# Kernel optimization log

Hardware: AMD Instinct MI355X
Metric: run time of the kernel (lower is better)

## Reference

```python
import jax, jax.numpy as jnp
import numpy as np

SCALE = 0.08838834764831845  # head_dim ** -0.5
NUM_HEADS = 32
NUM_KV_HEADS = 8
HEAD_DIM = 128
PAGE_SIZE = 16


def setup_inputs() -> dict:
    key = jax.random.key(0)
    k1, k2 = jax.random.split(key)
    B = 32
    L0_PAGES = 256        # shared prefix: 4096 tokens
    L1_PAGES = 64         # per-seq chunk: 1024 tokens
    L2_PAGES = 32         # per-seq suffix: 512 tokens
    P = L0_PAGES + B * L1_PAGES + B * L2_PAGES  # 3328 pages
    q = jax.random.normal(k1, (B, NUM_HEADS * HEAD_DIM), jnp.float32)
    # paged KV cache, layout [page, k/v, page_size, kv_heads, head_dim]
    kv_cache = jax.random.normal(k2, (P, 2, PAGE_SIZE, NUM_KV_HEADS, HEAD_DIM), jnp.float32)
    shared_page_idx = jnp.arange(L0_PAGES, dtype=jnp.int32)
    seq1_page_idx = (L0_PAGES + jnp.arange(B * L1_PAGES, dtype=jnp.int32)).reshape(B, L1_PAGES)
    seq2_page_idx = (L0_PAGES + B * L1_PAGES + jnp.arange(B * L2_PAGES, dtype=jnp.int32)).reshape(B, L2_PAGES)
    return {"q": q, "kv_cache": kv_cache, "shared_page_idx": shared_page_idx,
            "seq1_page_idx": seq1_page_idx, "seq2_page_idx": seq2_page_idx}


def _softmax_attn(scores, V, av_eq):
    # scores: [..., L]; returns (out, lse) with a single stable pass
    m = scores.max(axis=-1, keepdims=True)
    e = jnp.exp(scores - m)
    denom = e.sum(axis=-1)
    out = jnp.einsum(av_eq, e, V) / denom[..., None]
    lse = m[..., 0] + jnp.log(denom)
    return out, lse


def _merge_state(oa, sa, ob, sb):
    # flashinfer.merge_state: LSE-weighted combination of attention states
    s = jnp.logaddexp(sa, sb)
    o = oa * jnp.exp(sa - s)[..., None] + ob * jnp.exp(sb - s)[..., None]
    return o, s


def _forward(q, kv_cache, shared_page_idx, seq1_page_idx, seq2_page_idx):
    B = q.shape[0]
    G = NUM_HEADS // NUM_KV_HEADS  # GQA group size = 4
    # q -> [B, Hkv, G, D]
    q4 = q.reshape(B, NUM_KV_HEADS, G, HEAD_DIM)

    # level 0: shared pages -> [L0, Hkv, D]
    K0 = kv_cache[shared_page_idx, 0].reshape(-1, NUM_KV_HEADS, HEAD_DIM)
    V0 = kv_cache[shared_page_idx, 1].reshape(-1, NUM_KV_HEADS, HEAD_DIM)
    s0 = jnp.einsum('bkgd,lkd->bkgl', q4, K0) * SCALE
    out, lse = _softmax_attn(s0, V0, 'bkgl,lkd->bkgd')

    # levels 1 and 2: per-sequence paged KV -> [B, Li, Hkv, D]
    for idx in (seq1_page_idx, seq2_page_idx):
        Ki = kv_cache[idx, 0].reshape(B, -1, NUM_KV_HEADS, HEAD_DIM)
        Vi = kv_cache[idx, 1].reshape(B, -1, NUM_KV_HEADS, HEAD_DIM)
        si = jnp.einsum('bkgd,blkd->bkgl', q4, Ki) * SCALE
        oi, li = _softmax_attn(si, Vi, 'bkgl,blkd->bkgd')
        out, lse = _merge_state(out, lse, oi, li)

    return out.reshape(B, NUM_HEADS * HEAD_DIM)


def reference(q, kv_cache, shared_page_idx, seq1_page_idx, seq2_page_idx):
    return _forward(q, kv_cache, shared_page_idx, seq1_page_idx, seq2_page_idx)
```

## Files before the change

### kernel.cpp

```cpp
#include <hip/hip_runtime.h>
#include <stdint.h>


namespace {
constexpr int kG = 4, kD = 128;
constexpr float kQS = 0.08838834764831845f * 1.4426950408889634f;
constexpr int kNChunk = 32;
constexpr int kNSplit = 3;
constexpr int kNSrc = kNChunk + kNSplit;
constexpr size_t kOParts = (size_t)kNSrc * 32 * 8 * 4 * 128;
constexpr size_t kMLB = kOParts;
constexpr size_t kWsFloats = kOParts + (size_t)kNSrc * 32 * 8 * 4 * 2;
}

__device__ __forceinline__ float wave_max(float v) {
#pragma unroll
    for (int off = 1; off < 64; off <<= 1) v = fmaxf(v, __shfl_xor(v, off));
    return v;
}
__device__ __forceinline__ float wave_sum(float v) {
#pragma unroll
    for (int off = 1; off < 64; off <<= 1) v += __shfl_xor(v, off);
    return v;
}
__device__ __forceinline__ int kslot(int s, int t) { return s ^ (t & 31); }
__device__ __forceinline__ int vslot(int s, int t) {
    return s ^ (((t << 1) & 31) | ((t >> 4) & 1));
}

__global__ __launch_bounds__(512, 2)
void l0_kernel(const float* __restrict__ q, const float* __restrict__ kv,
               const int* __restrict__ sp0, float* __restrict__ ws)
{
    __shared__ __align__(16) float q_lds[32 * kG * kD];
    __shared__ __align__(16) float buf[2 * 64 * kD];
    __shared__ int pgs[8];

    const int h = blockIdx.x & 7;
    const int chunk = blockIdx.x >> 3;
    const int tid = threadIdx.x;
    const int w = tid >> 6, lane = tid & 63;

    {
        const int j0 = tid * 32;
        const int b = j0 >> 9, r = j0 & 511;
        const float4* src = (const float4*)(q + (size_t)b * 4096 + h * 512 + r);
        float4* dst = (float4*)&q_lds[j0];
#pragma unroll
        for (int u = 0; u < 8; ++u) {
            float4 v = src[u];
            v.x *= kQS; v.y *= kQS; v.z *= kQS; v.w *= kQS;
            dst[u] = v;
        }
    }
    if (tid < 8) pgs[tid] = sp0[chunk * 8 + tid];

    for (int pass = 0; pass < 2; ++pass) {
        float m[8], l[8], acc[8][8];
#pragma unroll
        for (int r = 0; r < 8; ++r) {
            m[r] = -1e30f; l[r] = 0.f;
#pragma unroll
            for (int e = 0; e < 8; ++e) acc[r][e] = 0.f;
        }

        for (int st = 0; st < 2; ++st) {
            __syncthreads();
            {
                const int t = tid >> 3;
                const int sg = (tid & 7) * 4;
                const int pg = pgs[st * 4 + (t >> 4)];
                const float* gk = kv + (size_t)pg * 32768 + (size_t)(t & 15) * 1024 + h * 128;
#pragma unroll
                for (int j = 0; j < 4; ++j) {
                    const int s = sg + j;
                    *(float4*)&buf[t * 128 + (kslot(s, t) << 2)] =
                        *(const float4*)(gk + s * 4);
                    *(float4*)&buf[8192 + t * 128 + (vslot(s, t) << 2)] =
                        *(const float4*)(gk + 16384 + s * 4);
                }
            }
            __syncthreads();

            const int sw = lane;
            float s[8] = {0.f,0.f,0.f,0.f,0.f,0.f,0.f,0.f};
#pragma unroll
            for (int c = 0; c < 16; ++c) {
                float4 ka = *(const float4*)&buf[lane * 128 + (kslot(2 * c, sw) << 2)];
                float4 kb = *(const float4*)&buf[lane * 128 + (kslot(2 * c + 1, sw) << 2)];
#pragma unroll
                for (int r = 0; r < 8; ++r) {
                    const int b = w * 4 + pass * 2 + (r >> 2);
                    const float* qp = &q_lds[(b * 4 + (r & 3)) * 128 + c * 8];
                    float4 qa = *(const float4*)qp;
                    float4 qb = *(const float4*)(qp + 4);
                    s[r] += ka.x * qa.x + ka.y * qa.y + ka.z * qa.z + ka.w * qa.w
                          + kb.x * qb.x + kb.y * qb.y + kb.z * qb.z + kb.w * qb.w;
                }
            }
            float p[8];
#pragma unroll
            for (int r = 0; r < 8; ++r) {
                float mt = wave_max(s[r]);
                float mn = fmaxf(m[r], mt);
                float alpha = exp2f(m[r] - mn);
                p[r] = exp2f(s[r] - mn);
                m[r] = mn;
                l[r] = l[r] * alpha + wave_sum(p[r]);
#pragma unroll
                for (int e = 0; e < 8; ++e) acc[r][e] *= alpha;
            }
            const int tq = lane >> 4, dg = lane & 15;
#pragma unroll
            for (int j = 0; j < 16; ++j) {
                const int t = tq * 16 + j;
                float4 va = *(const float4*)&buf[8192 + t * 128 + (vslot(2 * dg, t) << 2)];
                float4 vb = *(const float4*)&buf[8192 + t * 128 + (vslot(2 * dg + 1, t) << 2)];
#pragma unroll
                for (int r = 0; r < 8; ++r) {
                    float pj = __shfl(p[r], t);
                    acc[r][0] = fmaf(pj, va.x, acc[r][0]);
                    acc[r][1] = fmaf(pj, va.y, acc[r][1]);
                    acc[r][2] = fmaf(pj, va.z, acc[r][2]);
                    acc[r][3] = fmaf(pj, va.w, acc[r][3]);
                    acc[r][4] = fmaf(pj, vb.x, acc[r][4]);
                    acc[r][5] = fmaf(pj, vb.y, acc[r][5]);
                    acc[r][6] = fmaf(pj, vb.z, acc[r][6]);
                    acc[r][7] = fmaf(pj, vb.w, acc[r][7]);
                }
            }
        }

#pragma unroll
        for (int r = 0; r < 8; ++r)
#pragma unroll
            for (int e = 0; e < 8; ++e) {
                float v = acc[r][e];
                v += __shfl_xor(v, 16);
                v += __shfl_xor(v, 32);
                acc[r][e] = v;
            }
        if (lane < 16) {
            const int dg = lane;
#pragma unroll
            for (int r = 0; r < 8; ++r) {
                const int b = w * 4 + pass * 2 + (r >> 2);
                const size_t ob = ((((size_t)chunk * 32 + b) * 8 + h) * 4 + (r & 3)) * 128 + dg * 8;
                *(float4*)&ws[ob]     = make_float4(acc[r][0], acc[r][1], acc[r][2], acc[r][3]);
                *(float4*)&ws[ob + 4] = make_float4(acc[r][4], acc[r][5], acc[r][6], acc[r][7]);
            }
        }
        if (lane == 0) {
#pragma unroll
            for (int r = 0; r < 8; ++r) {
                const int b = w * 4 + pass * 2 + (r >> 2);
                const size_t idx = (((size_t)chunk * 32 + b) * 8 + h) * 4 + (r & 3);
                ws[kMLB + 2 * idx] = m[r];
                ws[kMLB + 2 * idx + 1] = l[r];
            }
        }
    }
}

__global__ __launch_bounds__(512, 4)
void seq_kernel(const float* __restrict__ q, const float* __restrict__ kv,
                const int* __restrict__ sp1, const int* __restrict__ sp2,
                float* __restrict__ ws)
{
    __shared__ __align__(16) float qs[kG * kD];
    __shared__ int plist[32];
    __shared__ __align__(16) float wacc[8][kG * kD];
    __shared__ float wm[8][kG], wl[8][kG];

    const int bid = blockIdx.x;
    const int split = bid >> 8;
    const int b = (bid & 255) >> 3;
    const int h = bid & 7;
    const int tid = threadIdx.x;

    {
        const int g = tid >> 7, d = tid & 127;
        qs[g * 128 + d] = q[(size_t)b * 4096 + h * 512 + g * 128 + d] * kQS;
    }
    if (tid < 32) {
        const int gi = split * 32 + tid;
        plist[tid] = (gi < 64) ? sp1[b * 64 + gi] : sp2[b * 32 + (gi - 64)];
    }
    __syncthreads();

    const int w = tid >> 6, lane = tid & 63;
    const int ts = lane >> 4, dg = lane & 15;
    const int page = plist[w * 4 + ts];
    const size_t poff = (size_t)page * 32768u;
    const float* Kp = kv + poff + (size_t)(lane & 15) * 1024u + h * 128;
    const float* Vp = kv + poff + 16384u + h * 128 + dg * 8;
    const float4* qv4 = (const float4*)qs;

    float s[kG] = {0.f, 0.f, 0.f, 0.f};
#pragma unroll
    for (int c = 0; c < 16; ++c) {
        float4 ka = *(const float4*)(Kp + c * 8);
        float4 kb = *(const float4*)(Kp + c * 8 + 4);
#pragma unroll
        for (int g = 0; g < kG; ++g) {
            float4 qa = qv4[g * 32 + c * 2];
            float4 qb = qv4[g * 32 + c * 2 + 1];
            s[g] += ka.x * qa.x + ka.y * qa.y + ka.z * qa.z + ka.w * qa.w
                  + kb.x * qb.x + kb.y * qb.y + kb.z * qb.z + kb.w * qb.w;
        }
    }
    float m[kG], p[kG], l[kG], acc[kG][8];
#pragma unroll
    for (int g = 0; g < kG; ++g) {
        m[g] = wave_max(s[g]);
        p[g] = exp2f(s[g] - m[g]);
        l[g] = wave_sum(p[g]);
#pragma unroll
        for (int e = 0; e < 8; ++e) acc[g][e] = 0.f;
    }
#pragma unroll
    for (int j = 0; j < 16; ++j) {
        const int t = ts * 16 + j;
        float4 va = *(const float4*)(Vp + (size_t)j * 1024u);
        float4 vb = *(const float4*)(Vp + (size_t)j * 1024u + 4);
#pragma unroll
        for (int g = 0; g < kG; ++g) {
            float pj = __shfl(p[g], t);
            acc[g][0] = fmaf(pj, va.x, acc[g][0]);
            acc[g][1] = fmaf(pj, va.y, acc[g][1]);
            acc[g][2] = fmaf(pj, va.z, acc[g][2]);
            acc[g][3] = fmaf(pj, va.w, acc[g][3]);
            acc[g][4] = fmaf(pj, vb.x, acc[g][4]);
            acc[g][5] = fmaf(pj, vb.y, acc[g][5]);
            acc[g][6] = fmaf(pj, vb.z, acc[g][6]);
            acc[g][7] = fmaf(pj, vb.w, acc[g][7]);
        }
    }
#pragma unroll
    for (int g = 0; g < kG; ++g)
#pragma unroll
        for (int e = 0; e < 8; ++e) {
            float v = acc[g][e];
            v += __shfl_xor(v, 16);
            v += __shfl_xor(v, 32);
            acc[g][e] = v;
        }
    if (lane < 16) {
#pragma unroll
        for (int g = 0; g < kG; ++g) {
            *(float4*)&wacc[w][g * 128 + dg * 8]     = make_float4(acc[g][0], acc[g][1], acc[g][2], acc[g][3]);
            *(float4*)&wacc[w][g * 128 + dg * 8 + 4] = make_float4(acc[g][4], acc[g][5], acc[g][6], acc[g][7]);
        }
        if (lane == 0)
#pragma unroll
            for (int g = 0; g < kG; ++g) { wm[w][g] = m[g]; wl[w][g] = l[g]; }
    }
    __syncthreads();

    {
        const int g = tid >> 7, d = tid & 127;
        float mstar = wm[0][g];
#pragma unroll
        for (int ww = 1; ww < 8; ++ww) mstar = fmaxf(mstar, wm[ww][g]);
        float numer = 0.f, denom = 0.f;
#pragma unroll
        for (int ww = 0; ww < 8; ++ww) {
            float sc = exp2f(wm[ww][g] - mstar);
            denom = fmaf(sc, wl[ww][g], denom);
            numer = fmaf(sc, wacc[ww][g * 128 + d], numer);
        }
        const size_t src = (size_t)(kNChunk + split);
        const size_t ob = (((src * 32 + b) * 8 + h) * 4 + g) * 128 + d;
        ws[ob] = numer;
        if (d == 0) {
            const size_t idx = ((src * 32 + b) * 8 + h) * 4 + g;
            ws[kMLB + 2 * idx] = mstar;
            ws[kMLB + 2 * idx + 1] = denom;
        }
    }
}

__global__ __launch_bounds__(512, 4)
void merge_kernel(const float* __restrict__ ws, float* __restrict__ out)
{
    __shared__ float sm[kNSrc][4], sl[kNSrc][4];
    const int b = blockIdx.x >> 3, h = blockIdx.x & 7;
    const int tid = threadIdx.x;
    if (tid < kNSrc * 4) {
        const int src = tid >> 2, g = tid & 3;
        const size_t idx = ((((size_t)src * 32 + b) * 8 + h) * 4 + g);
        sm[src][g] = ws[kMLB + 2 * idx];
        sl[src][g] = ws[kMLB + 2 * idx + 1];
    }
    __syncthreads();
    const int g = tid >> 7, d = tid & 127;
    float mstar = -1e30f;
#pragma unroll
    for (int s = 0; s < kNSrc; ++s) mstar = fmaxf(mstar, sm[s][g]);
    float numer = 0.f, denom = 0.f;
#pragma unroll 7
    for (int s = 0; s < kNSrc; ++s) {
        const float sc = exp2f(sm[s][g] - mstar);
        denom = fmaf(sc, sl[s][g], denom);
        const size_t ob = ((((size_t)s * 32 + b) * 8 + h) * 4 + g) * 128 + d;
        numer = fmaf(sc, ws[ob], numer);
    }
    out[(size_t)b * 4096 + h * 512 + g * 128 + d] = numer / denom;
}

__global__ __launch_bounds__(512, 2)
void fallback_kernel(const float* __restrict__ q, const float* __restrict__ kv,
                     const int* __restrict__ sp0, const int* __restrict__ sp1,
                     const int* __restrict__ sp2, float* __restrict__ out)
{
    __shared__ __align__(16) float qs[kG * kD];
    __shared__ int plist[352];
    __shared__ __align__(16) float wacc[8][kG * kD];
    __shared__ float wm[8][kG], wl[8][kG];
    const int b = blockIdx.x >> 3, h = blockIdx.x & 7;
    const int tid = threadIdx.x;
    {
        const int g = tid >> 7, d = tid & 127;
        qs[g * 128 + d] = q[(size_t)b * 4096 + h * 512 + g * 128 + d] * kQS;
    }
    if (tid < 352) {
        int pg;
        if (tid < 256)      pg = sp0[tid];
        else if (tid < 320) pg = sp1[b * 64 + (tid - 256)];
        else                pg = sp2[b * 32 + (tid - 320)];
        plist[tid] = pg;
    }
    __syncthreads();
    const int w = tid >> 6, lane = tid & 63;
    const int ts = lane >> 4, dg = lane & 15;
    const float4* qv4 = (const float4*)qs;
    float m[kG], l[kG], acc[kG][8];
#pragma unroll
    for (int g = 0; g < kG; ++g) {
        m[g] = -1e30f; l[g] = 0.f;
#pragma unroll
        for (int e = 0; e < 8; ++e) acc[g][e] = 0.f;
    }
    for (int tile = 0; tile < 11; ++tile) {
        const int page = plist[w * 44 + tile * 4 + ts];
        const size_t poff = (size_t)page * 32768u;
        const float* Kp = kv + poff + (size_t)(lane & 15) * 1024u + h * 128;
        const float* Vp = kv + poff + 16384u + h * 128 + dg * 8;
        float s[kG] = {0.f, 0.f, 0.f, 0.f};
#pragma unroll
        for (int c = 0; c < 16; ++c) {
            float4 ka = *(const float4*)(Kp + c * 8);
            float4 kb = *(const float4*)(Kp + c * 8 + 4);
#pragma unroll
            for (int g = 0; g < kG; ++g) {
                float4 qa = qv4[g * 32 + c * 2];
                float4 qb = qv4[g * 32 + c * 2 + 1];
                s[g] += ka.x * qa.x + ka.y * qa.y + ka.z * qa.z + ka.w * qa.w
                      + kb.x * qb.x + kb.y * qb.y + kb.z * qb.z + kb.w * qb.w;
            }
        }
        float p[kG];
#pragma unroll
        for (int g = 0; g < kG; ++g) {
            float mt = wave_max(s[g]);
            float mn = fmaxf(m[g], mt);
            float alpha = exp2f(m[g] - mn);
            p[g] = exp2f(s[g] - mn);
            m[g] = mn;
            l[g] = l[g] * alpha + wave_sum(p[g]);
#pragma unroll
            for (int e = 0; e < 8; ++e) acc[g][e] *= alpha;
        }
#pragma unroll
        for (int j = 0; j < 16; ++j) {
            const int t = ts * 16 + j;
            float4 va = *(const float4*)(Vp + (size_t)j * 1024u);
            float4 vb = *(const float4*)(Vp + (size_t)j * 1024u + 4);
#pragma unroll
            for (int g = 0; g < kG; ++g) {
                float pj = __shfl(p[g], t);
                acc[g][0] = fmaf(pj, va.x, acc[g][0]);
                acc[g][1] = fmaf(pj, va.y, acc[g][1]);
                acc[g][2] = fmaf(pj, va.z, acc[g][2]);
                acc[g][3] = fmaf(pj, va.w, acc[g][3]);
                acc[g][4] = fmaf(pj, vb.x, acc[g][4]);
                acc[g][5] = fmaf(pj, vb.y, acc[g][5]);
                acc[g][6] = fmaf(pj, vb.z, acc[g][6]);
                acc[g][7] = fmaf(pj, vb.w, acc[g][7]);
            }
        }
    }
#pragma unroll
    for (int g = 0; g < kG; ++g)
#pragma unroll
        for (int e = 0; e < 8; ++e) {
            float v = acc[g][e];
            v += __shfl_xor(v, 16);
            v += __shfl_xor(v, 32);
            acc[g][e] = v;
        }
    if (lane < 16) {
#pragma unroll
        for (int g = 0; g < kG; ++g) {
            *(float4*)&wacc[w][g * 128 + dg * 8]     = make_float4(acc[g][0], acc[g][1], acc[g][2], acc[g][3]);
            *(float4*)&wacc[w][g * 128 + dg * 8 + 4] = make_float4(acc[g][4], acc[g][5], acc[g][6], acc[g][7]);
        }
        if (lane == 0)
#pragma unroll
            for (int g = 0; g < kG; ++g) { wm[w][g] = m[g]; wl[w][g] = l[g]; }
    }
    __syncthreads();
    {
        const int g = tid >> 7, d = tid & 127;
        float mstar = wm[0][g];
#pragma unroll
        for (int ww = 1; ww < 8; ++ww) mstar = fmaxf(mstar, wm[ww][g]);
        float numer = 0.f, denom = 0.f;
#pragma unroll
        for (int ww = 0; ww < 8; ++ww) {
            float sc = exp2f(wm[ww][g] - mstar);
            denom = fmaf(sc, wl[ww][g], denom);
            numer = fmaf(sc, wacc[ww][g * 128 + d], numer);
        }
        out[(size_t)b * 4096 + h * 512 + g * 128 + d] = numer / denom;
    }
}

extern "C" void kernel_launch(void* const* d_in, const int* in_sizes, int n_in,
                              void* d_out, int out_size, void* d_ws, size_t ws_size,
                              hipStream_t stream) {
    const float* q  = (const float*)d_in[0];
    const float* kv = (const float*)d_in[1];
    const int* sp0 = (const int*)d_in[2];
    const int* sp1 = (const int*)d_in[3];
    const int* sp2 = (const int*)d_in[4];
    float* out = (float*)d_out;
    float* ws = (float*)d_ws;
    if (ws_size >= kWsFloats * sizeof(float)) {
        hipLaunchKernelGGL(l0_kernel,    dim3(256), dim3(512), 0, stream, q, kv, sp0, ws);
        hipLaunchKernelGGL(seq_kernel,   dim3(768), dim3(512), 0, stream, q, kv, sp1, sp2, ws);
        hipLaunchKernelGGL(merge_kernel, dim3(256), dim3(512), 0, stream, ws, out);
    } else {
        hipLaunchKernelGGL(fallback_kernel, dim3(256), dim3(512), 0, stream,
                           q, kv, sp0, sp1, sp2, out);
    }
}
```

Before: 690.0 us.

## Fuse shared-prefix and per-sequence attention into one interleaved kernel launch

Combines the level-0 shared-prefix kernel and the per-sequence split kernel into a single 1280-block launch, interleaving two prefix blocks with three sequence blocks in every group of five. Each prefix block now handles 4 pages instead of 8, doubling the chunk count to 64. Queries are read straight from global memory rather than staged in LDS, and the scale is applied after the dot product. The aim is to drop one launch, let the two workloads overlap on the CUs and raise occupancy. In exchange the merge kernel has more partial states to combine and the workspace grows.

```diff
diff --git a/kernel.cpp b/kernel.cpp
--- a/kernel.cpp
+++ b/kernel.cpp
@@ -5,7 +5,7 @@
 namespace {
 constexpr int kG = 4, kD = 128;
 constexpr float kQS = 0.08838834764831845f * 1.4426950408889634f;
-constexpr int kNChunk = 32;
+constexpr int kNChunk = 64;
 constexpr int kNSplit = 3;
 constexpr int kNSrc = kNChunk + kNSplit;
 constexpr size_t kOParts = (size_t)kNSrc * 32 * 8 * 4 * 128;
@@ -28,254 +28,220 @@
     return s ^ (((t << 1) & 31) | ((t >> 4) & 1));
 }
 
-__global__ __launch_bounds__(512, 2)
-void l0_kernel(const float* __restrict__ q, const float* __restrict__ kv,
-               const int* __restrict__ sp0, float* __restrict__ ws)
+__global__ __launch_bounds__(512, 4)
+void fused_kernel(const float* __restrict__ q, const float* __restrict__ kv,
+                  const int* __restrict__ sp0, const int* __restrict__ sp1,
+                  const int* __restrict__ sp2, float* __restrict__ ws)
 {
-    __shared__ __align__(16) float q_lds[32 * kG * kD];
-    __shared__ __align__(16) float buf[2 * 64 * kD];
-    __shared__ int pgs[8];
-
-    const int h = blockIdx.x & 7;
-    const int chunk = blockIdx.x >> 3;
+    __shared__ __align__(16) float smem[16384];
+    __shared__ int pgs[4];
+
+    const int bid = blockIdx.x;
+    const int grp = bid / 5, rem = bid % 5;
     const int tid = threadIdx.x;
     const int w = tid >> 6, lane = tid & 63;
-
-    {
-        const int j0 = tid * 32;
-        const int b = j0 >> 9, r = j0 & 511;
-        const float4* src = (const float4*)(q + (size_t)b * 4096 + h * 512 + r);
-        float4* dst = (float4*)&q_lds[j0];
-#pragma unroll
-        for (int u = 0; u < 8; ++u) {
-            float4 v = src[u];
-            v.x *= kQS; v.y *= kQS; v.z *= kQS; v.w *= kQS;
-            dst[u] = v;
-        }
-    }
-    if (tid < 8) pgs[tid] = sp0[chunk * 8 + tid];
-
-    for (int pass = 0; pass < 2; ++pass) {
-        float m[8], l[8], acc[8][8];
-#pragma unroll
-        for (int r = 0; r < 8; ++r) {
-            m[r] = -1e30f; l[r] = 0.f;
-#pragma unroll
-            for (int e = 0; e < 8; ++e) acc[r][e] = 0.f;
-        }
-
-        for (int st = 0; st < 2; ++st) {
-            __syncthreads();
-            {
-                const int t = tid >> 3;
-                const int sg = (tid & 7) * 4;
-                const int pg = pgs[st * 4 + (t >> 4)];
-                const float* gk = kv + (size_t)pg * 32768 + (size_t)(t & 15) * 1024 + h * 128;
-#pragma unroll
-                for (int j = 0; j < 4; ++j) {
-                    const int s = sg + j;
-                    *(float4*)&buf[t * 128 + (kslot(s, t) << 2)] =
-                        *(const float4*)(gk + s * 4);
-                    *(float4*)&buf[8192 + t * 128 + (vslot(s, t) << 2)] =
-                        *(const float4*)(gk + 16384 + s * 4);
+    const int ts = lane >> 4, dg = lane & 15;
+
+    if (rem < 2) {
+        const int lid = grp * 2 + rem;
+        const int h = lid & 7, c4 = lid >> 3;
+        if (tid < 4) pgs[tid] = sp0[c4 * 4 + tid];
+        __syncthreads();
+        {
+            const int t = tid >> 3;
+            const int sg = (tid & 7) * 4;
+            const int pg = pgs[t >> 4];
+            const float* gk = kv + (size_t)pg * 32768u + (size_t)(t & 15) * 1024u + h * 128;
+#pragma unroll
+            for (int j = 0; j < 4; ++j) {
+                const int s = sg + j;
+                *(float4*)&smem[t * 128 + (kslot(s, t) << 2)] =
+                    *(const float4*)(gk + s * 4);
+                *(float4*)&smem[8192 + t * 128 + (vslot(s, t) << 2)] =
+                    *(const float4*)(gk + 16384 + s * 4);
+            }
+        }
+        __syncthreads();
+
+        const int wq = __builtin_amdgcn_readfirstlane(w);
+        for (int pass = 0; pass < 4; ++pass) {
+            const int b = wq * 4 + pass;
+            const float* qb = q + (size_t)b * 4096 + h * 512;
+            float s[4] = {0.f, 0.f, 0.f, 0.f};
+#pragma unroll
+            for (int c = 0; c < 16; ++c) {
+                float4 ka = *(const float4*)&smem[lane * 128 + (kslot(2 * c, lane) << 2)];
+                float4 kb = *(const float4*)&smem[lane * 128 + (kslot(2 * c + 1, lane) << 2)];
+#pragma unroll
+                for (int g = 0; g < 4; ++g) {
+                    float4 qa = *(const float4*)(qb + g * 128 + c * 8);
+                    float4 q2 = *(const float4*)(qb + g * 128 + c * 8 + 4);
+                    s[g] += ka.x * qa.x + ka.y * qa.y + ka.z * qa.z + ka.w * qa.w
+                          + kb.x * q2.x + kb.y * q2.y + kb.z * q2.z + kb.w * q2.w;
                 }
             }
-            __syncthreads();
-
-            const int sw = lane;
-            float s[8] = {0.f,0.f,0.f,0.f,0.f,0.f,0.f,0.f};
-#pragma unroll
-            for (int c = 0; c < 16; ++c) {
-                float4 ka = *(const float4*)&buf[lane * 128 + (kslot(2 * c, sw) << 2)];
-                float4 kb = *(const float4*)&buf[lane * 128 + (kslot(2 * c + 1, sw) << 2)];
-#pragma unroll
-                for (int r = 0; r < 8; ++r) {
-                    const int b = w * 4 + pass * 2 + (r >> 2);
-                    const float* qp = &q_lds[(b * 4 + (r & 3)) * 128 + c * 8];
-                    float4 qa = *(const float4*)qp;
-                    float4 qb = *(const float4*)(qp + 4);
-                    s[r] += ka.x * qa.x + ka.y * qa.y + ka.z * qa.z + ka.w * qa.w
-                          + kb.x * qb.x + kb.y * qb.y + kb.z * qb.z + kb.w * qb.w;
+            float m[4], p[4], l[4], acc[4][8];
+#pragma unroll
+            for (int g = 0; g < 4; ++g) {
+                s[g] *= kQS;
+                m[g] = wave_max(s[g]);
+                p[g] = exp2f(s[g] - m[g]);
+                l[g] = wave_sum(p[g]);
+#pragma unroll
+                for (int e = 0; e < 8; ++e) acc[g][e] = 0.f;
+            }
+#pragma unroll
+            for (int j = 0; j < 16; ++j) {
+                const int t = ts * 16 + j;
+                float4 va = *(const float4*)&smem[8192 + t * 128 + (vslot(2 * dg, t) << 2)];
+                float4 vb = *(const float4*)&smem[8192 + t * 128 + (vslot(2 * dg + 1, t) << 2)];
+#pragma unroll
+                for (int g = 0; g < 4; ++g) {
+                    float pj = __shfl(p[g], t);
+                    acc[g][0] = fmaf(pj, va.x, acc[g][0]);
+                    acc[g][1] = fmaf(pj, va.y, acc[g][1]);
+                    acc[g][2] = fmaf(pj, va.z, acc[g][2]);
+                    acc[g][3] = fmaf(pj, va.w, acc[g][3]);
+                    acc[g][4] = fmaf(pj, vb.x, acc[g][4]);
+                    acc[g][5] = fmaf(pj, vb.y, acc[g][5]);
+                    acc[g][6] = fmaf(pj, vb.z, acc[g][6]);
+                    acc[g][7] = fmaf(pj, vb.w, acc[g][7]);
                 }
             }
-            float p[8];
-#pragma unroll
-            for (int r = 0; r < 8; ++r) {
-                float mt = wave_max(s[r]);
-                float mn = fmaxf(m[r], mt);
-                float alpha = exp2f(m[r] - mn);
-                p[r] = exp2f(s[r] - mn);
-                m[r] = mn;
-                l[r] = l[r] * alpha + wave_sum(p[r]);
-#pragma unroll
-                for (int e = 0; e < 8; ++e) acc[r][e] *= alpha;
-            }
-            const int tq = lane >> 4, dg = lane & 15;
-#pragma unroll
-            for (int j = 0; j < 16; ++j) {
-                const int t = tq * 16 + j;
-                float4 va = *(const float4*)&buf[8192 + t * 128 + (vslot(2 * dg, t) << 2)];
-                float4 vb = *(const float4*)&buf[8192 + t * 128 + (vslot(2 * dg + 1, t) << 2)];
-#pragma unroll
-                for (int r = 0; r < 8; ++r) {
-                    float pj = __shfl(p[r], t);
-                    acc[r][0] = fmaf(pj, va.x, acc[r][0]);
-                    acc[r][1] = fmaf(pj, va.y, acc[r][1]);
-                    acc[r][2] = fmaf(pj, va.z, acc[r][2]);
-                    acc[r][3] = fmaf(pj, va.w, acc[r][3]);
-                    acc[r][4] = fmaf(pj, vb.x, acc[r][4]);
-                    acc[r][5] = fmaf(pj, vb.y, acc[r][5]);
-                    acc[r][6] = fmaf(pj, vb.z, acc[r][6]);
-                    acc[r][7] = fmaf(pj, vb.w, acc[r][7]);
+#pragma unroll
+            for (int g = 0; g < 4; ++g)
+#pragma unroll
+                for (int e = 0; e < 8; ++e) {
+                    float v = acc[g][e];
+                    v += __shfl_xor(v, 16);
+                    v += __shfl_xor(v, 32);
+                    acc[g][e] = v;
                 }
-            }
-        }
-
-#pragma unroll
-        for (int r = 0; r < 8; ++r)
+            if (lane < 16) {
+                const size_t ob = ((((size_t)c4 * 32 + b) * 8 + h) * 4) * 128 + lane * 8;
+#pragma unroll
+                for (int g = 0; g < 4; ++g) {
+                    *(float4*)&ws[ob + (size_t)g * 128] =
+                        make_float4(acc[g][0], acc[g][1], acc[g][2], acc[g][3]);
+                    *(float4*)&ws[ob + (size_t)g * 128 + 4] =
+                        make_float4(acc[g][4], acc[g][5], acc[g][6], acc[g][7]);
+                }
+            }
+            if (lane == 0) {
+                const size_t idx = (((size_t)c4 * 32 + b) * 8 + h) * 4;
+#pragma unroll
+                for (int g = 0; g < 4; ++g) {
+                    ws[kMLB + 2 * (idx + g)] = m[g];
+                    ws[kMLB + 2 * (idx + g) + 1] = l[g];
+                }
+            }
+        }
+    } else {
+        const int sid = grp * 3 + (rem - 2);
+        const int split = sid >> 8;
+        const int b = (sid & 255) >> 3;
+        const int h = sid & 7;
+        float* wacc = smem;
+        float* wm = smem + 4096;
+        float* wl = smem + 4128;
+        int* plist = (int*)(smem + 4160);
+
+        if (tid < 32) {
+            const int gi = split * 32 + tid;
+            plist[tid] = (gi < 64) ? sp1[b * 64 + gi] : sp2[b * 32 + (gi - 64)];
+        }
+        __syncthreads();
+
+        const int page = plist[w * 4 + ts];
+        const size_t poff = (size_t)page * 32768u;
+        const float* Kp = kv + poff + (size_t)(lane & 15) * 1024u + h * 128;
+        const float* Vp = kv + poff + 16384u + h * 128 + dg * 8;
+        const float* qb = q + (size_t)b * 4096 + h * 512;
+
+        float s[kG] = {0.f, 0.f, 0.f, 0.f};
+#pragma unroll
+        for (int c = 0; c < 16; ++c) {
+            float4 ka = *(const float4*)(Kp + c * 8);
+            float4 kb = *(const float4*)(Kp + c * 8 + 4);
+#pragma unroll
+            for (int g = 0; g < kG; ++g) {
+                float4 qa = *(const float4*)(qb + g * 128 + c * 8);
+                float4 q2 = *(const float4*)(qb + g * 128 + c * 8 + 4);
+                s[g] += ka.x * qa.x + ka.y * qa.y + ka.z * qa.z + ka.w * qa.w
+                      + kb.x * q2.x + kb.y * q2.y + kb.z * q2.z + kb.w * q2.w;
+            }
+        }
+        float m[kG], p[kG], l[kG], acc[kG][8];
+#pragma unroll
+        for (int g = 0; g < kG; ++g) {
+            s[g] *= kQS;
+            m[g] = wave_max(s[g]);
+            p[g] = exp2f(s[g] - m[g]);
+            l[g] = wave_sum(p[g]);
+#pragma unroll
+            for (int e = 0; e < 8; ++e) acc[g][e] = 0.f;
+        }
+#pragma unroll
+        for (int j = 0; j < 16; ++j) {
+            const int t = ts * 16 + j;
+            float4 va = *(const float4*)(Vp + (size_t)j * 1024u);
+            float4 vb = *(const float4*)(Vp + (size_t)j * 1024u + 4);
+#pragma unroll
+            for (int g = 0; g < kG; ++g) {
+                float pj = __shfl(p[g], t);
+                acc[g][0] = fmaf(pj, va.x, acc[g][0]);
+                acc[g][1] = fmaf(pj, va.y, acc[g][1]);
+                acc[g][2] = fmaf(pj, va.z, acc[g][2]);
+                acc[g][3] = fmaf(pj, va.w, acc[g][3]);
+                acc[g][4] = fmaf(pj, vb.x, acc[g][4]);
+                acc[g][5] = fmaf(pj, vb.y, acc[g][5]);
+                acc[g][6] = fmaf(pj, vb.z, acc[g][6]);
+                acc[g][7] = fmaf(pj, vb.w, acc[g][7]);
+            }
+        }
+#pragma unroll
+        for (int g = 0; g < kG; ++g)
 #pragma unroll
             for (int e = 0; e < 8; ++e) {
-                float v = acc[r][e];
+                float v = acc[g][e];
                 v += __shfl_xor(v, 16);
                 v += __shfl_xor(v, 32);
-                acc[r][e] = v;
+                acc[g][e] = v;
             }
         if (lane < 16) {
-            const int dg = lane;
-#pragma unroll
-            for (int r = 0; r < 8; ++r) {
-                const int b = w * 4 + pass * 2 + (r >> 2);
-                const size_t ob = ((((size_t)chunk * 32 + b) * 8 + h) * 4 + (r & 3)) * 128 + dg * 8;
-                *(float4*)&ws[ob]     = make_float4(acc[r][0], acc[r][1], acc[r][2], acc[r][3]);
-                *(float4*)&ws[ob + 4] = make_float4(acc[r][4], acc[r][5], acc[r][6], acc[r][7]);
-            }
-        }
-        if (lane == 0) {
-#pragma unroll
-            for (int r = 0; r < 8; ++r) {
-                const int b = w * 4 + pass * 2 + (r >> 2);
-                const size_t idx = (((size_t)chunk * 32 + b) * 8 + h) * 4 + (r & 3);
-                ws[kMLB + 2 * idx] = m[r];
-                ws[kMLB + 2 * idx + 1] = l[r];
-            }
-        }
-    }
-}
-
-__global__ __launch_bounds__(512, 4)
-void seq_kernel(const float* __restrict__ q, const float* __restrict__ kv,
-                const int* __restrict__ sp1, const int* __restrict__ sp2,
-                float* __restrict__ ws)
-{
-    __shared__ __align__(16) float qs[kG * kD];
-    __shared__ int plist[32];
-    __shared__ __align__(16) float wacc[8][kG * kD];
-    __shared__ float wm[8][kG], wl[8][kG];
-
-    const int bid = blockIdx.x;
-    const int split = bid >> 8;
-    const int b = (bid & 255) >> 3;
-    const int h = bid & 7;
-    const int tid = threadIdx.x;
-
-    {
-        const int g = tid >> 7, d = tid & 127;
-        qs[g * 128 + d] = q[(size_t)b * 4096 + h * 512 + g * 128 + d] * kQS;
-    }
-    if (tid < 32) {
-        const int gi = split * 32 + tid;
-        plist[tid] = (gi < 64) ? sp1[b * 64 + gi] : sp2[b * 32 + (gi - 64)];
-    }
-    __syncthreads();
-
-    const int w = tid >> 6, lane = tid & 63;
-    const int ts = lane >> 4, dg = lane & 15;
-    const int page = plist[w * 4 + ts];
-    const size_t poff = (size_t)page * 32768u;
-    const float* Kp = kv + poff + (size_t)(lane & 15) * 1024u + h * 128;
-    const float* Vp = kv + poff + 16384u + h * 128 + dg * 8;
-    const float4* qv4 = (const float4*)qs;
-
-    float s[kG] = {0.f, 0.f, 0.f, 0.f};
-#pragma unroll
-    for (int c = 0; c < 16; ++c) {
-        float4 ka = *(const float4*)(Kp + c * 8);
-        float4 kb = *(const float4*)(Kp + c * 8 + 4);
-#pragma unroll
-        for (int g = 0; g < kG; ++g) {
-            float4 qa = qv4[g * 32 + c * 2];
-            float4 qb = qv4[g * 32 + c * 2 + 1];
-            s[g] += ka.x * qa.x + ka.y * qa.y + ka.z * qa.z + ka.w * qa.w
-                  + kb.x * qb.x + kb.y * qb.y + kb.z * qb.z + kb.w * qb.w;
-        }
-    }
-    float m[kG], p[kG], l[kG], acc[kG][8];
-#pragma unroll
-    for (int g = 0; g < kG; ++g) {
-        m[g] = wave_max(s[g]);
-        p[g] = exp2f(s[g] - m[g]);
-        l[g] = wave_sum(p[g]);
-#pragma unroll
-        for (int e = 0; e < 8; ++e) acc[g][e] = 0.f;
-    }
-#pragma unroll
-    for (int j = 0; j < 16; ++j) {
-        const int t = ts * 16 + j;
-        float4 va = *(const float4*)(Vp + (size_t)j * 1024u);
-        float4 vb = *(const float4*)(Vp + (size_t)j * 1024u + 4);
-#pragma unroll
-        for (int g = 0; g < kG; ++g) {
-            float pj = __shfl(p[g], t);
-            acc[g][0] = fmaf(pj, va.x, acc[g][0]);
-            acc[g][1] = fmaf(pj, va.y, acc[g][1]);
-            acc[g][2] = fmaf(pj, va.z, acc[g][2]);
-            acc[g][3] = fmaf(pj, va.w, acc[g][3]);
-            acc[g][4] = fmaf(pj, vb.x, acc[g][4]);
-            acc[g][5] = fmaf(pj, vb.y, acc[g][5]);
-            acc[g][6] = fmaf(pj, vb.z, acc[g][6]);
-            acc[g][7] = fmaf(pj, vb.w, acc[g][7]);
-        }
-    }
-#pragma unroll
-    for (int g = 0; g < kG; ++g)
-#pragma unroll
-        for (int e = 0; e < 8; ++e) {
-            float v = acc[g][e];
-            v += __shfl_xor(v, 16);
-            v += __shfl_xor(v, 32);
-            acc[g][e] = v;
-        }
-    if (lane < 16) {
-#pragma unroll
-        for (int g = 0; g < kG; ++g) {
-            *(float4*)&wacc[w][g * 128 + dg * 8]     = make_float4(acc[g][0], acc[g][1], acc[g][2], acc[g][3]);
-            *(float4*)&wacc[w][g * 128 + dg * 8 + 4] = make_float4(acc[g][4], acc[g][5], acc[g][6], acc[g][7]);
-        }
-        if (lane == 0)
-#pragma unroll
-            for (int g = 0; g < kG; ++g) { wm[w][g] = m[g]; wl[w][g] = l[g]; }
-    }
-    __syncthreads();
-
-    {
-        const int g = tid >> 7, d = tid & 127;
-        float mstar = wm[0][g];
-#pragma unroll
-        for (int ww = 1; ww < 8; ++ww) mstar = fmaxf(mstar, wm[ww][g]);
-        float numer = 0.f, denom = 0.f;
-#pragma unroll
-        for (int ww = 0; ww < 8; ++ww) {
-            float sc = exp2f(wm[ww][g] - mstar);
-            denom = fmaf(sc, wl[ww][g], denom);
-            numer = fmaf(sc, wacc[ww][g * 128 + d], numer);
-        }
-        const size_t src = (size_t)(kNChunk + split);
-        const size_t ob = (((src * 32 + b) * 8 + h) * 4 + g) * 128 + d;
-        ws[ob] = numer;
-        if (d == 0) {
-            const size_t idx = ((src * 32 + b) * 8 + h) * 4 + g;
-            ws[kMLB + 2 * idx] = mstar;
-            ws[kMLB + 2 * idx + 1] = denom;
+#pragma unroll
+            for (int g = 0; g < kG; ++g) {
+                *(float4*)&wacc[w * 512 + g * 128 + dg * 8] =
+                    make_float4(acc[g][0], acc[g][1], acc[g][2], acc[g][3]);
+                *(float4*)&wacc[w * 512 + g * 128 + dg * 8 + 4] =
+                    make_float4(acc[g][4], acc[g][5], acc[g][6], acc[g][7]);
+            }
+            if (lane == 0)
+#pragma unroll
+                for (int g = 0; g < kG; ++g) { wm[w * 4 + g] = m[g]; wl[w * 4 + g] = l[g]; }
+        }
+        __syncthreads();
+
+        {
+            const int g = tid >> 7, d = tid & 127;
+            float mstar = wm[g];
+#pragma unroll
+            for (int ww = 1; ww < 8; ++ww) mstar = fmaxf(mstar, wm[ww * 4 + g]);
+            float numer = 0.f, denom = 0.f;
+#pragma unroll
+            for (int ww = 0; ww < 8; ++ww) {
+                float sc = exp2f(wm[ww * 4 + g] - mstar);
+                denom = fmaf(sc, wl[ww * 4 + g], denom);
+                numer = fmaf(sc, wacc[ww * 512 + g * 128 + d], numer);
+            }
+            const size_t src = (size_t)(kNChunk + split);
+            const size_t ob = (((src * 32 + b) * 8 + h) * 4 + g) * 128 + d;
+            ws[ob] = numer;
+            if (d == 0) {
+                const size_t idx = ((src * 32 + b) * 8 + h) * 4 + g;
+                ws[kMLB + 2 * idx] = mstar;
+                ws[kMLB + 2 * idx + 1] = denom;
+            }
         }
     }
 }
@@ -298,7 +264,7 @@
 #pragma unroll
     for (int s = 0; s < kNSrc; ++s) mstar = fmaxf(mstar, sm[s][g]);
     float numer = 0.f, denom = 0.f;
-#pragma unroll 7
+#pragma unroll 4
     for (int s = 0; s < kNSrc; ++s) {
         const float sc = exp2f(sm[s][g] - mstar);
         denom = fmaf(sc, sl[s][g], denom);
@@ -437,8 +403,8 @@
     float* out = (float*)d_out;
     float* ws = (float*)d_ws;
     if (ws_size >= kWsFloats * sizeof(float)) {
-        hipLaunchKernelGGL(l0_kernel,    dim3(256), dim3(512), 0, stream, q, kv, sp0, ws);
-        hipLaunchKernelGGL(seq_kernel,   dim3(768), dim3(512), 0, stream, q, kv, sp1, sp2, ws);
+        hipLaunchKernelGGL(fused_kernel, dim3(1280), dim3(512), 0, stream,
+                           q, kv, sp0, sp1, sp2, ws);
         hipLaunchKernelGGL(merge_kernel, dim3(256), dim3(512), 0, stream, ws, out);
     } else {
         hipLaunchKernelGGL(fallback_kernel, dim3(256), dim3(512), 0, stream,
```

After: 911.0 us. +32.0%, slower.
